# Performance work log

Hardware: AMD Instinct MI355X
Metric: run time of the kernel (lower is better)

Reference implementation:

```python
import jax, jax.numpy as jnp
import numpy as np

BN_EPS = 1e-5
N_NODES = 100000
N_EDGES = 300000
IN_FEAT = 256
HIDDEN = 128
N_ETYPES = 4


def setup_inputs() -> dict:
    key = jax.random.key(0)
    ks = jax.random.split(key, 10)
    s = 1.0 / np.sqrt(2 * IN_FEAT)
    return {
        "h_src": jax.random.normal(ks[0], (N_NODES, IN_FEAT), jnp.float32),
        "h_dst": jax.random.normal(ks[1], (N_NODES, IN_FEAT), jnp.float32),
        "src_nodes": jax.random.randint(ks[2], (N_EDGES,), 0, N_NODES),
        "dst_nodes": jax.random.randint(ks[3], (N_EDGES,), 0, N_NODES),
        "etype_idx": 0,
        "W1": jax.random.normal(ks[4], (2 * IN_FEAT, HIDDEN), jnp.float32) * s,
        "b1": jnp.zeros((HIDDEN,), jnp.float32),
        "bn_gamma": jnp.ones((HIDDEN,), jnp.float32),
        "bn_beta": jnp.zeros((HIDDEN,), jnp.float32),
        "bn_mean": jnp.zeros((HIDDEN,), jnp.float32),
        "bn_var": jnp.ones((HIDDEN,), jnp.float32),
        "emb": jax.random.normal(ks[5], (N_ETYPES, HIDDEN), jnp.float32),
        "W2": jax.random.normal(ks[6], (HIDDEN, HIDDEN // 2), jnp.float32) * (1.0 / np.sqrt(HIDDEN)),
        "b2": jnp.zeros((HIDDEN // 2,), jnp.float32),
        "W3": jax.random.normal(ks[7], (HIDDEN // 2, 1), jnp.float32) * (1.0 / np.sqrt(HIDDEN // 2)),
        "b3": jnp.zeros((1,), jnp.float32),
    }


def reference(h_src, h_dst, src_nodes, dst_nodes, etype_idx,
              W1, b1, bn_gamma, bn_beta, bn_mean, bn_var,
              emb, W2, b2, W3, b3):
    # gather endpoint features and concat -> [E, 2*in_feat]
    src_feat = h_src[src_nodes]
    dst_feat = h_dst[dst_nodes]
    edge_feat = jnp.concatenate([src_feat, dst_feat], axis=1)
    # Linear + ReLU (Dropout is identity in eval) + BatchNorm1d (running stats)
    x = jax.nn.relu(edge_feat @ W1 + b1)
    x = (x - bn_mean) * jax.lax.rsqrt(bn_var + BN_EPS) * bn_gamma + bn_beta
    # add edge-type embedding (broadcast over edges)
    x = x + emb[etype_idx]
    # per-edge-type predictor MLP -> scalar score per edge
    x = jax.nn.relu(x @ W2 + b2)
    scores = (x @ W3 + b3).squeeze(-1)
    return scores
```

## Files before the change

kernel.cpp:

```cpp
#include <hip/hip_runtime.h>
#include <hip/hip_bf16.h>


typedef __attribute__((ext_vector_type(8))) short bf16x8;
typedef __attribute__((ext_vector_type(4))) float f32x4;

constexpr int HID   = 128;
constexpr int ETILE = 64;
constexpr int AS    = 72;
constexpr int XS    = 136;

__device__ inline ushort f2bf(float f) {
    union { __hip_bfloat16 h; ushort u; } cv;
    cv.h = __float2bfloat16(f);
    return cv.u;
}

__global__ __launch_bounds__(256)
void prep_kernel(const float* __restrict__ W1, const float* __restrict__ W2,
                 const float* __restrict__ bn_gamma, const float* __restrict__ bn_beta,
                 const float* __restrict__ bn_mean, const float* __restrict__ bn_var,
                 const float* __restrict__ emb, const int* __restrict__ etype,
                 ushort* __restrict__ B1p, ushort* __restrict__ B2p,
                 float* __restrict__ sc, float* __restrict__ sh)
{
    int i = blockIdx.x * blockDim.x + threadIdx.x;
    if (i < 65536) {
        int j = i & 7, lane = (i >> 3) & 63, ct = (i >> 9) & 7, ks = i >> 12;
        int k = ks * 32 + (lane >> 4) * 8 + j;
        int c = ct * 16 + (lane & 15);
        B1p[i] = f2bf(W1[k * HID + c]);
    } else if (i < 65536 + 8192) {
        int p = i - 65536;
        int j = p & 7, lane = (p >> 3) & 63, ct = (p >> 9) & 3, ks = p >> 11;
        int k = ks * 32 + (lane >> 4) * 8 + j;
        int c = ct * 16 + (lane & 15);
        B2p[p] = f2bf(W2[k * 64 + c]);
    } else if (i < 65536 + 8192 + HID) {
        int c = i - 65536 - 8192;
        float s = bn_gamma[c] * rsqrtf(bn_var[c] + 1e-5f);
        sc[c] = s;
        sh[c] = bn_beta[c] - bn_mean[c] * s + emb[etype[0] * HID + c];
    }
}

__global__ __launch_bounds__(256, 4)
void edge_mlp_mfma(const float* __restrict__ h_src, const float* __restrict__ h_dst,
                   const int* __restrict__ src_nodes, const int* __restrict__ dst_nodes,
                   const ushort* __restrict__ B1p, const ushort* __restrict__ B2p,
                   const float* __restrict__ b1, const float* __restrict__ sc,
                   const float* __restrict__ sh, const float* __restrict__ b2,
                   const float* __restrict__ W3, const float* __restrict__ b3,
                   float* __restrict__ out, int n_edges)
{
    __shared__ ushort sA[2][ETILE * AS];
    __shared__ int s_src[ETILE], s_dst[ETILE];

    const int t    = threadIdx.x;
    const int lane = t & 63;
    const int w    = t >> 6;
    const int lr   = lane & 15;
    const int lq   = lane >> 4;
    const int ebase = blockIdx.x * ETILE;

    if (t < ETILE) {
        int e = ebase + t;
        s_src[t] = src_nodes[e < n_edges ? e : 0];
    } else if (t < 2 * ETILE) {
        int e = ebase + t - ETILE;
        s_dst[t - ETILE] = dst_nodes[e < n_edges ? e : 0];
    }

    f32x4 acc[4][2];
#pragma unroll
    for (int rt = 0; rt < 4; ++rt)
#pragma unroll
        for (int c = 0; c < 2; ++c) acc[rt][c] = (f32x4)0.0f;

    float4 rA[4], rB[4];

#define LOADC(kc, R) do {                                                      \
        const float* hp = ((kc) < 4) ? h_src : h_dst;                          \
        const int* sidx = ((kc) < 4) ? s_src : s_dst;                          \
        const int koff = ((kc) & 3) * 64;                                      \
        _Pragma("unroll")                                                      \
        for (int i = 0; i < 4; ++i) {                                          \
            int f = t + i * 256; int e = f >> 4; int q = f & 15;               \
            R[i] = *reinterpret_cast<const float4*>(                           \
                hp + (size_t)sidx[e] * 256 + koff + q * 4);                    \
        } } while (0)

#define STOREC(B, R) do {                                                      \
        _Pragma("unroll")                                                      \
        for (int i = 0; i < 4; ++i) {                                          \
            int f = t + i * 256; int e = f >> 4; int q = f & 15;               \
            ushort4 bv;                                                        \
            bv.x = f2bf(R[i].x); bv.y = f2bf(R[i].y);                          \
            bv.z = f2bf(R[i].z); bv.w = f2bf(R[i].w);                          \
            *reinterpret_cast<ushort4*>(&sA[B][e * AS + q * 4]) = bv;          \
        } } while (0)

#define COMP(kc, B) do {                                                       \
        _Pragma("unroll")                                                      \
        for (int ks = 0; ks < 2; ++ks) {                                       \
            const int kstep = (kc) * 2 + ks;                                   \
            bf16x8 bf0 = *reinterpret_cast<const bf16x8*>(                     \
                B1p + (size_t)(((kstep * 8) + 2 * w) * 64 + lane) * 8);        \
            bf16x8 bf1 = *reinterpret_cast<const bf16x8*>(                     \
                B1p + (size_t)(((kstep * 8) + 2 * w + 1) * 64 + lane) * 8);    \
            _Pragma("unroll")                                                  \
            for (int rt = 0; rt < 4; ++rt) {                                   \
                bf16x8 af = *reinterpret_cast<const bf16x8*>(                  \
                    &sA[B][(rt * 16 + lr) * AS + ks * 32 + lq * 8]);           \
                acc[rt][0] = __builtin_amdgcn_mfma_f32_16x16x32_bf16(af, bf0, acc[rt][0], 0, 0, 0); \
                acc[rt][1] = __builtin_amdgcn_mfma_f32_16x16x32_bf16(af, bf1, acc[rt][1], 0, 0, 0); \
            } } } while (0)

    __syncthreads();
    LOADC(0, rA);
    STOREC(0, rA);
    LOADC(1, rB);
    __syncthreads();

    LOADC(2, rA);  COMP(0, 0);  STOREC(1, rB);  __syncthreads();
    LOADC(3, rB);  COMP(1, 1);  STOREC(0, rA);  __syncthreads();
    LOADC(4, rA);  COMP(2, 0);  STOREC(1, rB);  __syncthreads();
    LOADC(5, rB);  COMP(3, 1);  STOREC(0, rA);  __syncthreads();
    LOADC(6, rA);  COMP(4, 0);  STOREC(1, rB);  __syncthreads();
    LOADC(7, rB);  COMP(5, 1);  STOREC(0, rA);  __syncthreads();
                   COMP(6, 0);  STOREC(1, rB);  __syncthreads();
                   COMP(7, 1);

#undef LOADC
#undef STOREC
#undef COMP

    __syncthreads();
    ushort* sX = &sA[0][0];
#pragma unroll
    for (int ctl = 0; ctl < 2; ++ctl) {
        int c = (2 * w + ctl) * 16 + lr;
        float bb = b1[c], s = sc[c], z = sh[c];
#pragma unroll
        for (int rt = 0; rt < 4; ++rt)
#pragma unroll
            for (int r = 0; r < 4; ++r) {
                float x = fmaxf(acc[rt][ctl][r] + bb, 0.0f);
                sX[(rt * 16 + lq * 4 + r) * XS + c] = f2bf(fmaf(x, s, z));
            }
    }
    __syncthreads();

    f32x4 acc2[4];
#pragma unroll
    for (int ct = 0; ct < 4; ++ct) acc2[ct] = (f32x4)0.0f;

#pragma unroll
    for (int ks = 0; ks < 4; ++ks) {
        bf16x8 af = *reinterpret_cast<const bf16x8*>(
            &sX[(w * 16 + lr) * XS + ks * 32 + lq * 8]);
#pragma unroll
        for (int ct = 0; ct < 4; ++ct) {
            bf16x8 bf = *reinterpret_cast<const bf16x8*>(
                B2p + (size_t)((ks * 4 + ct) * 64 + lane) * 8);
            acc2[ct] = __builtin_amdgcn_mfma_f32_16x16x32_bf16(af, bf, acc2[ct], 0, 0, 0);
        }
    }

    float w3v[4], b2v[4];
#pragma unroll
    for (int ct = 0; ct < 4; ++ct) {
        int c = ct * 16 + lr;
        w3v[ct] = W3[c];
        b2v[ct] = b2[c];
    }
#pragma unroll
    for (int r = 0; r < 4; ++r) {
        float sum = 0.0f;
#pragma unroll
        for (int ct = 0; ct < 4; ++ct)
            sum += fmaxf(acc2[ct][r] + b2v[ct], 0.0f) * w3v[ct];
        sum += __shfl_xor(sum, 1);
        sum += __shfl_xor(sum, 2);
        sum += __shfl_xor(sum, 4);
        sum += __shfl_xor(sum, 8);
        int e = ebase + w * 16 + lq * 4 + r;
        if (lr == 0 && e < n_edges) out[e] = sum + b3[0];
    }
}

extern "C" void kernel_launch(void* const* d_in, const int* in_sizes, int n_in,
                              void* d_out, int out_size, void* d_ws, size_t ws_size,
                              hipStream_t stream) {
    const float* h_src     = (const float*)d_in[0];
    const float* h_dst     = (const float*)d_in[1];
    const int*   src_nodes = (const int*)d_in[2];
    const int*   dst_nodes = (const int*)d_in[3];
    const int*   etype     = (const int*)d_in[4];
    const float* W1        = (const float*)d_in[5];
    const float* b1        = (const float*)d_in[6];
    const float* bn_gamma  = (const float*)d_in[7];
    const float* bn_beta   = (const float*)d_in[8];
    const float* bn_mean   = (const float*)d_in[9];
    const float* bn_var    = (const float*)d_in[10];
    const float* emb       = (const float*)d_in[11];
    const float* W2        = (const float*)d_in[12];
    const float* b2        = (const float*)d_in[13];
    const float* W3        = (const float*)d_in[14];
    const float* b3        = (const float*)d_in[15];

    ushort* B1p = (ushort*)d_ws;
    ushort* B2p = B1p + 65536;
    float*  scp = (float*)(B2p + 8192);
    float*  shp = scp + HID;

    prep_kernel<<<(65536 + 8192 + HID + 255) / 256, 256, 0, stream>>>(
        W1, W2, bn_gamma, bn_beta, bn_mean, bn_var, emb, etype, B1p, B2p, scp, shp);

    const int n_edges = in_sizes[2];
    const int grid = (n_edges + ETILE - 1) / ETILE;
    edge_mlp_mfma<<<grid, 256, 0, stream>>>(h_src, h_dst, src_nodes, dst_nodes,
                                            B1p, B2p, b1, scp, shp, b2, W3, b3,
                                            (float*)d_out, n_edges);
}
```

Before: 102.9 us.

## Prefetch W1 fragments one phase ahead and use LDS-only barriers

```diff
diff --git a/kernel.cpp b/kernel.cpp
--- a/kernel.cpp
+++ b/kernel.cpp
@@ -78,6 +78,12 @@
         for (int c = 0; c < 2; ++c) acc[rt][c] = (f32x4)0.0f;
 
     float4 rA[4], rB[4];
+    bf16x8 Bf0[4], Bf1[4];
+
+#define PHASE_BAR() do {                                                       \
+        asm volatile("s_waitcnt lgkmcnt(0)" ::: "memory");                     \
+        __builtin_amdgcn_s_barrier();                                          \
+    } while (0)
 
 #define LOADC(kc, R) do {                                                      \
         const float* hp = ((kc) < 4) ? h_src : h_dst;                          \
@@ -89,6 +95,15 @@
             R[i] = *reinterpret_cast<const float4*>(                           \
                 hp + (size_t)sidx[e] * 256 + koff + q * 4);                    \
         } } while (0)
+
+#define BLOAD(kc, BR) do {                                                     \
+        _Pragma("unroll")                                                      \
+        for (int s = 0; s < 2; ++s)                                            \
+        _Pragma("unroll")                                                      \
+        for (int c = 0; c < 2; ++c)                                            \
+            BR[s * 2 + c] = *reinterpret_cast<const bf16x8*>(                  \
+                B1p + (size_t)((((kc) * 2 + s) * 8 + 2 * w + c) * 64 + lane) * 8); \
+        } while (0)
 
 #define STOREC(B, R) do {                                                      \
         _Pragma("unroll")                                                      \
@@ -100,40 +115,40 @@
             *reinterpret_cast<ushort4*>(&sA[B][e * AS + q * 4]) = bv;          \
         } } while (0)
 
-#define COMP(kc, B) do {                                                       \
+#define COMP(B, BR) do {                                                       \
         _Pragma("unroll")                                                      \
         for (int ks = 0; ks < 2; ++ks) {                                       \
-            const int kstep = (kc) * 2 + ks;                                   \
-            bf16x8 bf0 = *reinterpret_cast<const bf16x8*>(                     \
-                B1p + (size_t)(((kstep * 8) + 2 * w) * 64 + lane) * 8);        \
-            bf16x8 bf1 = *reinterpret_cast<const bf16x8*>(                     \
-                B1p + (size_t)(((kstep * 8) + 2 * w + 1) * 64 + lane) * 8);    \
             _Pragma("unroll")                                                  \
             for (int rt = 0; rt < 4; ++rt) {                                   \
                 bf16x8 af = *reinterpret_cast<const bf16x8*>(                  \
                     &sA[B][(rt * 16 + lr) * AS + ks * 32 + lq * 8]);           \
-                acc[rt][0] = __builtin_amdgcn_mfma_f32_16x16x32_bf16(af, bf0, acc[rt][0], 0, 0, 0); \
-                acc[rt][1] = __builtin_amdgcn_mfma_f32_16x16x32_bf16(af, bf1, acc[rt][1], 0, 0, 0); \
+                acc[rt][0] = __builtin_amdgcn_mfma_f32_16x16x32_bf16(af, BR[ks * 2 + 0], acc[rt][0], 0, 0, 0); \
+                acc[rt][1] = __builtin_amdgcn_mfma_f32_16x16x32_bf16(af, BR[ks * 2 + 1], acc[rt][1], 0, 0, 0); \
             } } } while (0)
 
     __syncthreads();
+
     LOADC(0, rA);
+    BLOAD(0, Bf0);
     STOREC(0, rA);
     LOADC(1, rB);
-    __syncthreads();
-
-    LOADC(2, rA);  COMP(0, 0);  STOREC(1, rB);  __syncthreads();
-    LOADC(3, rB);  COMP(1, 1);  STOREC(0, rA);  __syncthreads();
-    LOADC(4, rA);  COMP(2, 0);  STOREC(1, rB);  __syncthreads();
-    LOADC(5, rB);  COMP(3, 1);  STOREC(0, rA);  __syncthreads();
-    LOADC(6, rA);  COMP(4, 0);  STOREC(1, rB);  __syncthreads();
-    LOADC(7, rB);  COMP(5, 1);  STOREC(0, rA);  __syncthreads();
-                   COMP(6, 0);  STOREC(1, rB);  __syncthreads();
-                   COMP(7, 1);
+    BLOAD(1, Bf1);
+    PHASE_BAR();
+
+    LOADC(2, rA);  COMP(0, Bf0);  BLOAD(2, Bf0);  STOREC(1, rB);  PHASE_BAR();
+    LOADC(3, rB);  COMP(1, Bf1);  BLOAD(3, Bf1);  STOREC(0, rA);  PHASE_BAR();
+    LOADC(4, rA);  COMP(0, Bf0);  BLOAD(4, Bf0);  STOREC(1, rB);  PHASE_BAR();
+    LOADC(5, rB);  COMP(1, Bf1);  BLOAD(5, Bf1);  STOREC(0, rA);  PHASE_BAR();
+    LOADC(6, rA);  COMP(0, Bf0);  BLOAD(6, Bf0);  STOREC(1, rB);  PHASE_BAR();
+    LOADC(7, rB);  COMP(1, Bf1);  BLOAD(7, Bf1);  STOREC(0, rA);  PHASE_BAR();
+                   COMP(0, Bf0);                  STOREC(1, rB);  PHASE_BAR();
+                   COMP(1, Bf1);
 
 #undef LOADC
+#undef BLOAD
 #undef STOREC
 #undef COMP
+#undef PHASE_BAR
 
     __syncthreads();
     ushort* sX = &sA[0][0];
```

New measurement: 97.02 us. 1.06x faster.
